# Performance work log

Hardware: AMD Instinct MI355X
Metric: run time of the kernel (lower is better)

Reference implementation:

```python
import jax, jax.numpy as jnp
import numpy as np

N_NODES = 50000


def gat_layer(x, src, dst, W, att_s, att_d, b, concat):
    # PyG GATConv (eval mode): h = x W reshaped to [N, H, C]
    H, C = att_s.shape
    h = (x @ W).reshape(-1, H, C)                      # [N, H, C]
    a_s = (h * att_s).sum(-1)                          # [N, H]
    a_d = (h * att_d).sum(-1)                          # [N, H]
    e = jax.nn.leaky_relu(a_s[src] + a_d[dst], 0.2)    # [E, H]
    # scatter-softmax over destination nodes
    m = jax.ops.segment_max(e, dst, num_segments=N_NODES)
    alpha = jnp.exp(e - m[dst])
    denom = jax.ops.segment_sum(alpha, dst, num_segments=N_NODES)
    alpha = alpha / denom[dst]                         # [E, H]
    msg = h[src] * alpha[:, :, None]                   # [E, H, C]
    out = jax.ops.segment_sum(msg, dst, num_segments=N_NODES)  # [N, H, C]
    out = out.reshape(N_NODES, H * C) if concat else out.mean(axis=1)
    return out + b


def setup_inputs() -> dict:
    key = jax.random.key(0)
    ks = jax.random.split(key, 16)
    F_IN, HID, HEADS, NCLS, E = 512, 64, 4, 40, 800000
    x = jax.random.normal(ks[0], (N_NODES, F_IN), dtype=jnp.float32)
    edge_index = jax.random.randint(ks[1], (2, E), 0, N_NODES, dtype=jnp.int32)

    def glorot(k, shape):
        fan = shape[0]
        return jax.random.normal(k, shape, dtype=jnp.float32) / np.sqrt(fan)

    d1 = HID * HEADS  # 256
    return {
        "x": x,
        "edge_index": edge_index,
        "W1": glorot(ks[2], (F_IN, d1)),
        "as1": glorot(ks[3], (HEADS, HID)),
        "ad1": glorot(ks[4], (HEADS, HID)),
        "b1": jnp.zeros((d1,), jnp.float32),
        "W2": glorot(ks[5], (d1, d1)),
        "as2": glorot(ks[6], (HEADS, HID)),
        "ad2": glorot(ks[7], (HEADS, HID)),
        "b2": jnp.zeros((d1,), jnp.float32),
        "W3": glorot(ks[8], (d1, NCLS)),
        "as3": glorot(ks[9], (1, NCLS)),
        "ad3": glorot(ks[10], (1, NCLS)),
        "b3": jnp.zeros((NCLS,), jnp.float32),
    }


def reference(x, edge_index, W1, as1, ad1, b1, W2, as2, ad2, b2, W3, as3, ad3, b3):
    # add self-loops (PyG GATConv default)
    loops = jnp.arange(N_NODES, dtype=edge_index.dtype)
    src = jnp.concatenate([edge_index[0], loops])
    dst = jnp.concatenate([edge_index[1], loops])
    h = jax.nn.elu(gat_layer(x, src, dst, W1, as1, ad1, b1, True))
    h = jax.nn.elu(gat_layer(h, src, dst, W2, as2, ad2, b2, True))
    out = gat_layer(h, src, dst, W3, as3, ad3, b3, False)
    return out
```

## Files before the change

kernel.cpp:

```cpp
#include <hip/hip_runtime.h>
#include <stdint.h>

#define NN 50000
#define NB 196

typedef unsigned short u16;
typedef _Float16 f16;
typedef __attribute__((ext_vector_type(8))) _Float16 half8;
typedef __attribute__((ext_vector_type(4))) _Float16 half4;
typedef __attribute__((ext_vector_type(4))) float f32x4;

__device__ __forceinline__ void gload_lds16(const void* gsrc, void* ldst){
  __builtin_amdgcn_global_load_lds(
      (const __attribute__((address_space(1))) unsigned int*)gsrc,
      (__attribute__((address_space(3))) unsigned int*)ldst,
      16, 0, 0);
}


__global__ void count_k(const int* __restrict__ dst, int* __restrict__ cnt, int E){
  int i = blockIdx.x * 256 + threadIdx.x;
  int tot = E + NN;
  if (i >= tot) return;
  int d = (i < E) ? dst[i] : (i - E);
  atomicAdd(&cnt[d], 1);
}

__global__ __launch_bounds__(256) void scan_part_k(const int* __restrict__ cnt,
                                                   int* __restrict__ bsum){
  __shared__ int lds[256];
  int tid = threadIdx.x;
  int idx = blockIdx.x * 256 + tid;
  lds[tid] = (idx < NN) ? cnt[idx] : 0;
  __syncthreads();
#pragma unroll
  for (int off = 128; off >= 1; off >>= 1){
    if (tid < off) lds[tid] += lds[tid + off];
    __syncthreads();
  }
  if (tid == 0) bsum[blockIdx.x] = lds[0];
}

__global__ __launch_bounds__(256) void scan_top_k(const int* __restrict__ bsum,
                                                  int* __restrict__ boff,
                                                  int* __restrict__ row_ptr){
  __shared__ int lds[256];
  int tid = threadIdx.x;
  int v = (tid < NB) ? bsum[tid] : 0;
  lds[tid] = v;
  __syncthreads();
#pragma unroll
  for (int off = 1; off < 256; off <<= 1){
    int t = (tid >= off) ? lds[tid - off] : 0;
    __syncthreads();
    lds[tid] += t;
    __syncthreads();
  }
  if (tid < NB) boff[tid] = lds[tid] - v;
  if (tid == 255) row_ptr[NN] = lds[255];
}

__global__ __launch_bounds__(256) void scan_fin_k(const int* __restrict__ cnt,
                                                  const int* __restrict__ boff,
                                                  int* __restrict__ row_ptr,
                                                  int* __restrict__ cursor){
  __shared__ int lds[256];
  int tid = threadIdx.x;
  int idx = blockIdx.x * 256 + tid;
  int v = (idx < NN) ? cnt[idx] : 0;
  lds[tid] = v;
  __syncthreads();
#pragma unroll
  for (int off = 1; off < 256; off <<= 1){
    int t = (tid >= off) ? lds[tid - off] : 0;
    __syncthreads();
    lds[tid] += t;
    __syncthreads();
  }
  if (idx < NN){
    int r = boff[blockIdx.x] + lds[tid] - v;
    row_ptr[idx] = r;
    cursor[idx]  = r;
  }
}

__global__ void scatter_k(const int* __restrict__ src, const int* __restrict__ dst,
                          int* __restrict__ cursor, int* __restrict__ csr, int E){
  int i = blockIdx.x * 256 + threadIdx.x;
  int tot = E + NN;
  if (i >= tot) return;
  int s, d;
  if (i < E){ s = src[i]; d = dst[i]; } else { s = i - E; d = i - E; }
  int pos = atomicAdd(&cursor[d], 1);
  csr[pos] = s;
}


__global__ void transpose_k(const float* __restrict__ W, f16* __restrict__ Wt, int K, int N){
  int i = blockIdx.x * 256 + threadIdx.x;
  if (i >= K * N) return;
  int n = i / K, k = i - n * K;
  Wt[i] = (f16)W[k * N + n];
}


template<bool A_FP32>
__global__ __launch_bounds__(256) void gemm_tile2_k(const void* __restrict__ Aptr,
                                                    const f16* __restrict__ Bt,
                                                    f16* __restrict__ C,
                                                    const float* __restrict__ atts,
                                                    const float* __restrict__ attd,
                                                    float* __restrict__ a_s,
                                                    float* __restrict__ a_d,
                                                    int M, int N, int K){
  constexpr int ABYTES = A_FP32 ? 16384 : 8192;
  constexpr int STEPB  = ABYTES + 8192;
  __shared__ __attribute__((aligned(16))) char lds[2 * STEPB];

  const int tid  = threadIdx.x;
  const int wave = tid >> 6, lane = tid & 63;
  const int quad = lane >> 4, l16 = lane & 15;
  const int wm = wave >> 1, wn = wave & 1;
  const int m0 = blockIdx.x * 128, n0 = blockIdx.y * 128;
  const int sc_l = lane >> 4, r_l = lane & 15;

  size_t bsrc[2]; int bdst[2];
#pragma unroll
  for (int j = 0; j < 2; ++j){
    int nt = wave * 2 + j;
    bsrc[j] = (size_t)(n0 + nt * 16 + r_l) * K + sc_l * 8;
    bdst[j] = (wave * 128 + j * 64) * 16;
  }
  size_t asrc[4]; int adst[4];
  if constexpr (A_FP32){
#pragma unroll
    for (int j = 0; j < 4; ++j){
      int mt = wave * 2 + (j & 1);
      int h  = j >> 1;
      int row = m0 + mt * 16 + r_l; if (row > M - 1) row = M - 1;
      asrc[j] = (size_t)row * K + sc_l * 8 + h * 4;
      adst[j] = h * 8192 + mt * 1024;
    }
  } else {
#pragma unroll
    for (int j = 0; j < 2; ++j){
      int mt = wave * 2 + j;
      int row = m0 + mt * 16 + r_l; if (row > M - 1) row = M - 1;
      asrc[j] = (size_t)row * K + sc_l * 8;
      adst[j] = mt * 1024;
      asrc[j + 2] = 0; adst[j + 2] = 0;
    }
  }

  auto stage = [&](int buf, int k0){
    char* Ab  = lds + buf * STEPB;
    char* Bb  = Ab + ABYTES;
    if constexpr (A_FP32){
      const float* A = (const float*)Aptr;
#pragma unroll
      for (int j = 0; j < 4; ++j)
        gload_lds16(A + asrc[j] + k0, Ab + adst[j]);
    } else {
      const f16* A = (const f16*)Aptr;
#pragma unroll
      for (int j = 0; j < 2; ++j)
        gload_lds16(A + asrc[j] + k0, Ab + adst[j]);
    }
#pragma unroll
    for (int j = 0; j < 2; ++j)
      gload_lds16(Bt + bsrc[j] + k0, Bb + bdst[j]);
  };

  f32x4 acc[4][4] = {};

  stage(0, 0);
  asm volatile("s_waitcnt vmcnt(0)" ::: "memory");
  __syncthreads();

  const int nk = K >> 5;
  int cur = 0;
  for (int t = 0; t < nk; ++t){
    if (t + 1 < nk) stage(cur ^ 1, (t + 1) << 5);

    char* Ab = lds + cur * STEPB;
    f16*  Bb = (f16*)(Ab + ABYTES);
    half8 af[4], bf[4];
    if constexpr (A_FP32){
#pragma unroll
      for (int i = 0; i < 4; ++i){
        const f32x4 lo = *(const f32x4*)(Ab + (((wm * 4 + i) * 64 + lane) * 16));
        const f32x4 hi = *(const f32x4*)(Ab + 8192 + (((wm * 4 + i) * 64 + lane) * 16));
        half8 v;
        v[0] = (f16)lo.x; v[1] = (f16)lo.y; v[2] = (f16)lo.z; v[3] = (f16)lo.w;
        v[4] = (f16)hi.x; v[5] = (f16)hi.y; v[6] = (f16)hi.z; v[7] = (f16)hi.w;
        af[i] = v;
      }
    } else {
#pragma unroll
      for (int i = 0; i < 4; ++i)
        af[i] = *(const half8*)(Ab + (((wm * 4 + i) * 64 + lane) * 16));
    }
#pragma unroll
    for (int j = 0; j < 4; ++j)
      bf[j] = *(const half8*)((char*)Bb + (((wn * 4 + j) * 64 + lane) * 16));
#pragma unroll
    for (int i = 0; i < 4; ++i)
#pragma unroll
      for (int j = 0; j < 4; ++j)
        acc[i][j] = __builtin_amdgcn_mfma_f32_16x16x32_f16(af[i], bf[j], acc[i][j], 0, 0, 0);

    __syncthreads();
    cur ^= 1;
  }

  const int head = blockIdx.y * 2 + wn;
  float sA[4], dA[4];
#pragma unroll
  for (int j = 0; j < 4; ++j){
    sA[j] = atts[head * 64 + j * 16 + l16];
    dA[j] = attd[head * 64 + j * 16 + l16];
  }
#pragma unroll
  for (int i = 0; i < 4; ++i){
#pragma unroll
    for (int r = 0; r < 4; ++r){
      int mm = m0 + (wm * 4 + i) * 16 + quad * 4 + r;
      float vs = 0.f, vd = 0.f;
#pragma unroll
      for (int j = 0; j < 4; ++j){
        float v = acc[i][j][r];
        vs += v * sA[j];
        vd += v * dA[j];
        int n = n0 + (wn * 4 + j) * 16 + l16;
        if (mm < M) C[(size_t)mm * N + n] = (f16)v;
      }
#pragma unroll
      for (int off = 8; off >= 1; off >>= 1){
        vs += __shfl_xor(vs, off);
        vd += __shfl_xor(vd, off);
      }
      if (l16 == 0 && mm < M){
        a_s[mm * 4 + head] = vs;
        a_d[mm * 4 + head] = vd;
      }
    }
  }
}


__global__ __launch_bounds__(256) void gemm_k(const f16* __restrict__ A,
                                              const f16* __restrict__ Bt,
                                              f16* __restrict__ C,
                                              const float* __restrict__ atts,
                                              const float* __restrict__ attd,
                                              float* __restrict__ a_s,
                                              float* __restrict__ a_d,
                                              int M, int N, int K){
  __shared__ f16 As[64 * 40];
  __shared__ f16 Bs[64 * 40];
  const int tid  = threadIdx.x;
  const int wave = tid >> 6, lane = tid & 63;
  const int quad = lane >> 4, l16 = lane & 15;
  const int m0 = blockIdx.x * 64, n0 = blockIdx.y * 64;
  const int srow = tid >> 2;
  const int scol = (tid & 3) * 8;

  f32x4 acc[4] = {};

  for (int k0 = 0; k0 < K; k0 += 32){
    half8 va = {0,0,0,0,0,0,0,0};
    int gm = m0 + srow;
    if (gm < M) va = *(const half8*)(A + (size_t)gm * K + k0 + scol);
    *(half8*)(&As[srow * 40 + scol]) = va;

    half8 vb = {0,0,0,0,0,0,0,0};
    int gn = n0 + srow;
    if (gn < N) vb = *(const half8*)(Bt + (size_t)gn * K + k0 + scol);
    *(half8*)(&Bs[srow * 40 + scol]) = vb;

    __syncthreads();
    half8 af = *(const half8*)(&As[(wave * 16 + l16) * 40 + quad * 8]);
#pragma unroll
    for (int i = 0; i < 4; i++){
      half8 bf = *(const half8*)(&Bs[(i * 16 + l16) * 40 + quad * 8]);
      acc[i] = __builtin_amdgcn_mfma_f32_16x16x32_f16(af, bf, acc[i], 0, 0, 0);
    }
    __syncthreads();
  }

#pragma unroll
  for (int i = 0; i < 4; i++){
    int n = n0 + i * 16 + l16;
#pragma unroll
    for (int r = 0; r < 4; r++){
      int m = m0 + wave * 16 + quad * 4 + r;
      if (m < M && n < N) C[(size_t)m * N + n] = (f16)acc[i][r];
    }
  }

  float sA[4], dA[4];
#pragma unroll
  for (int i = 0; i < 4; i++){
    int n = n0 + i * 16 + l16;
    sA[i] = (n < N) ? atts[n] : 0.f;
    dA[i] = (n < N) ? attd[n] : 0.f;
  }
#pragma unroll
  for (int r = 0; r < 4; r++){
    float vs = 0.f, vd = 0.f;
#pragma unroll
    for (int i = 0; i < 4; i++){
      vs += acc[i][r] * sA[i];
      vd += acc[i][r] * dA[i];
    }
#pragma unroll
    for (int off = 8; off >= 1; off >>= 1){
      vs += __shfl_xor(vs, off);
      vd += __shfl_xor(vd, off);
    }
    int m = m0 + wave * 16 + quad * 4 + r;
    if (l16 == 0 && m < M){
      a_s[m] = vs;
      a_d[m] = vd;
    }
  }
}


__device__ __forceinline__ float lrelu(float e){ return e > 0.f ? e : 0.2f * e; }

__global__ __launch_bounds__(256) void agg4_k(const f16* __restrict__ h,
                                              const float* __restrict__ a_s,
                                              const float* __restrict__ a_d,
                                              const int* __restrict__ row_ptr,
                                              const int* __restrict__ csr,
                                              const float* __restrict__ bias,
                                              f16* __restrict__ out){
  int w = blockIdx.x * 4 + (threadIdx.x >> 6);
  if (w >= NN) return;
  int lane = threadIdx.x & 63;
  int head = lane >> 4;
  float ad = a_d[w * 4 + head];
  int beg = row_ptr[w], end = row_ptr[w + 1];

  float m = -1e30f, denom = 0.f;
  float acc0 = 0.f, acc1 = 0.f, acc2 = 0.f, acc3 = 0.f;

  int s0 = csr[beg];
  int s1 = csr[(beg + 1 < end) ? beg + 1 : beg];
  float e0 = a_s[s0 * 4 + head];
  float e1 = a_s[s1 * 4 + head];
  half4 h0 = *(const half4*)(h + (size_t)s0 * 256 + lane * 4);
  half4 h1 = *(const half4*)(h + (size_t)s1 * 256 + lane * 4);

  for (int j = beg; j < end; j += 2){
    int t0 = (j + 2 < end) ? j + 2 : j;
    int t1 = (j + 3 < end) ? j + 3 : j;
    int sp0 = csr[t0], sp1 = csr[t1];
    float ep0 = a_s[sp0 * 4 + head];
    float ep1 = a_s[sp1 * 4 + head];
    half4 hp0 = *(const half4*)(h + (size_t)sp0 * 256 + lane * 4);
    half4 hp1 = *(const half4*)(h + (size_t)sp1 * 256 + lane * 4);

    float ee0 = lrelu(e0 + ad);
    float ee1 = (j + 1 < end) ? lrelu(e1 + ad) : -1e30f;
    float mn = fmaxf(m, fmaxf(ee0, ee1));
    float cold = __expf(m - mn);
    float al0 = __expf(ee0 - mn);
    float al1 = __expf(ee1 - mn);
    denom = denom * cold + al0 + al1;
    acc0 = acc0 * cold + al0 * (float)h0.x + al1 * (float)h1.x;
    acc1 = acc1 * cold + al0 * (float)h0.y + al1 * (float)h1.y;
    acc2 = acc2 * cold + al0 * (float)h0.z + al1 * (float)h1.z;
    acc3 = acc3 * cold + al0 * (float)h0.w + al1 * (float)h1.w;
    m = mn;
    e0 = ep0; e1 = ep1; h0 = hp0; h1 = hp1;
  }

  float inv = 1.f / fmaxf(denom, 1e-30f);
  float o0 = acc0 * inv + bias[lane * 4 + 0];
  float o1 = acc1 * inv + bias[lane * 4 + 1];
  float o2 = acc2 * inv + bias[lane * 4 + 2];
  float o3 = acc3 * inv + bias[lane * 4 + 3];
  o0 = o0 > 0.f ? o0 : __expf(o0) - 1.f;
  o1 = o1 > 0.f ? o1 : __expf(o1) - 1.f;
  o2 = o2 > 0.f ? o2 : __expf(o2) - 1.f;
  o3 = o3 > 0.f ? o3 : __expf(o3) - 1.f;
  half4 r; r.x = (f16)o0; r.y = (f16)o1; r.z = (f16)o2; r.w = (f16)o3;
  *(half4*)(out + (size_t)w * 256 + lane * 4) = r;
}

__global__ __launch_bounds__(256) void agg1_k(const f16* __restrict__ h,
                                              const float* __restrict__ a_s,
                                              const float* __restrict__ a_d,
                                              const int* __restrict__ row_ptr,
                                              const int* __restrict__ csr,
                                              const float* __restrict__ bias,
                                              float* __restrict__ out){
  int w = blockIdx.x * 4 + (threadIdx.x >> 6);
  if (w >= NN) return;
  int lane = threadIdx.x & 63;
  int cl = (lane < 40) ? lane : 0;
  float ad = a_d[w];
  int beg = row_ptr[w], end = row_ptr[w + 1];

  float m = -1e30f, denom = 0.f, acc = 0.f;

  int s0 = csr[beg];
  int s1 = csr[(beg + 1 < end) ? beg + 1 : beg];
  float e0 = a_s[s0];
  float e1 = a_s[s1];
  float h0 = (float)h[(size_t)s0 * 40 + cl];
  float h1 = (float)h[(size_t)s1 * 40 + cl];

  for (int j = beg; j < end; j += 2){
    int t0 = (j + 2 < end) ? j + 2 : j;
    int t1 = (j + 3 < end) ? j + 3 : j;
    int sp0 = csr[t0], sp1 = csr[t1];
    float ep0 = a_s[sp0];
    float ep1 = a_s[sp1];
    float hp0 = (float)h[(size_t)sp0 * 40 + cl];
    float hp1 = (float)h[(size_t)sp1 * 40 + cl];

    float ee0 = lrelu(e0 + ad);
    float ee1 = (j + 1 < end) ? lrelu(e1 + ad) : -1e30f;
    float mn = fmaxf(m, fmaxf(ee0, ee1));
    float cold = __expf(m - mn);
    float al0 = __expf(ee0 - mn);
    float al1 = __expf(ee1 - mn);
    denom = denom * cold + al0 + al1;
    acc = acc * cold + al0 * h0 + al1 * h1;
    m = mn;
    e0 = ep0; e1 = ep1; h0 = hp0; h1 = hp1;
  }

  if (lane < 40){
    float o = acc / fmaxf(denom, 1e-30f) + bias[lane];
    out[(size_t)w * 40 + lane] = o;
  }
}


extern "C" void kernel_launch(void* const* d_in, const int* in_sizes, int n_in,
                              void* d_out, int out_size, void* d_ws, size_t ws_size,
                              hipStream_t stream){
  const float* x   = (const float*)d_in[0];
  const int*   ei  = (const int*)d_in[1];
  const float* W1  = (const float*)d_in[2];
  const float* as1 = (const float*)d_in[3];
  const float* ad1 = (const float*)d_in[4];
  const float* b1  = (const float*)d_in[5];
  const float* W2  = (const float*)d_in[6];
  const float* as2 = (const float*)d_in[7];
  const float* ad2 = (const float*)d_in[8];
  const float* b2  = (const float*)d_in[9];
  const float* W3  = (const float*)d_in[10];
  const float* as3 = (const float*)d_in[11];
  const float* ad3 = (const float*)d_in[12];
  const float* b3  = (const float*)d_in[13];

  const int E = in_sizes[1] / 2;
  const int ETOT = E + NN;
  const int* src_arr = ei;
  const int* dst_arr = ei + E;

  char* ws = (char*)d_ws;
  size_t off = 0;
  auto alloc = [&](size_t bytes) -> void* {
    void* p = ws + off; off += (bytes + 255) & ~(size_t)255; return p;
  };
  int*   cnt     = (int*)  alloc((size_t)NN * 4);
  int*   row_ptr = (int*)  alloc((size_t)(NN + 1) * 4);
  int*   cursor  = (int*)  alloc((size_t)NN * 4);
  int*   csr     = (int*)  alloc((size_t)ETOT * 4);
  int*   bsum    = (int*)  alloc((size_t)256 * 4);
  int*   boff    = (int*)  alloc((size_t)256 * 4);
  f16*   W1t     = (f16*)  alloc((size_t)512 * 256 * 2);
  f16*   W2t     = (f16*)  alloc((size_t)256 * 256 * 2);
  f16*   W3t     = (f16*)  alloc((size_t)256 * 40 * 2);
  float* a_s     = (float*)alloc((size_t)NN * 4 * 4);
  float* a_d     = (float*)alloc((size_t)NN * 4 * 4);
  f16*   hbuf    = (f16*)  alloc((size_t)NN * 256 * 2);
  f16*   xbuf    = (f16*)  alloc((size_t)NN * 256 * 2);
  (void)ws_size; (void)n_in; (void)out_size;

  hipMemsetAsync(cnt, 0, (size_t)NN * 4, stream);
  int egrid = (ETOT + 255) / 256;
  count_k    <<<egrid, 256, 0, stream>>>(dst_arr, cnt, E);
  scan_part_k<<<NB, 256, 0, stream>>>(cnt, bsum);
  scan_top_k <<<1, 256, 0, stream>>>(bsum, boff, row_ptr);
  scan_fin_k <<<NB, 256, 0, stream>>>(cnt, boff, row_ptr, cursor);
  scatter_k  <<<egrid, 256, 0, stream>>>(src_arr, dst_arr, cursor, csr, E);

  transpose_k<<<(512 * 256 + 255) / 256, 256, 0, stream>>>(W1, W1t, 512, 256);
  transpose_k<<<(256 * 256 + 255) / 256, 256, 0, stream>>>(W2, W2t, 256, 256);
  transpose_k<<<(256 * 40  + 255) / 256, 256, 0, stream>>>(W3, W3t, 256, 40);

  dim3 blk(256);
  dim3 gT((NN + 127) / 128, 2);
  dim3 gC((NN + 63) / 64, 1);
  int nodeblocks = (NN + 3) / 4;

  gemm_tile2_k<true> <<<gT, blk, 0, stream>>>(x, W1t, hbuf, as1, ad1, a_s, a_d, NN, 256, 512);
  agg4_k <<<nodeblocks, blk, 0, stream>>>(hbuf, a_s, a_d, row_ptr, csr, b1, xbuf);

  gemm_tile2_k<false><<<gT, blk, 0, stream>>>(xbuf, W2t, hbuf, as2, ad2, a_s, a_d, NN, 256, 256);
  agg4_k <<<nodeblocks, blk, 0, stream>>>(hbuf, a_s, a_d, row_ptr, csr, b2, xbuf);

  gemm_k<<<gC, blk, 0, stream>>>(xbuf, W3t, hbuf, as3, ad3, a_s, a_d, NN, 40, 256);
  agg1_k <<<nodeblocks, blk, 0, stream>>>(hbuf, a_s, a_d, row_ptr, csr, b3, (float*)d_out);
}
```

Baseline: 549.7 us.

## Retile GEMMs, add pipelined N=40 GEMM, drop online max in aggregation

After: 534.1 us. 2.8% less time.

```diff
diff --git a/kernel.cpp b/kernel.cpp
--- a/kernel.cpp
+++ b/kernel.cpp
@@ -105,7 +105,7 @@
 
 
 template<bool A_FP32>
-__global__ __launch_bounds__(256) void gemm_tile2_k(const void* __restrict__ Aptr,
+__global__ __launch_bounds__(512) void gemm_tile3_k(const void* __restrict__ Aptr,
                                                     const f16* __restrict__ Bt,
                                                     f16* __restrict__ C,
                                                     const float* __restrict__ atts,
@@ -113,7 +113,7 @@
                                                     float* __restrict__ a_s,
                                                     float* __restrict__ a_d,
                                                     int M, int N, int K){
-  constexpr int ABYTES = A_FP32 ? 16384 : 8192;
+  constexpr int ABYTES = A_FP32 ? 8192 : 4096;
   constexpr int STEPB  = ABYTES + 8192;
   __shared__ __attribute__((aligned(16))) char lds[2 * STEPB];
 
@@ -121,57 +121,38 @@
   const int wave = tid >> 6, lane = tid & 63;
   const int quad = lane >> 4, l16 = lane & 15;
   const int wm = wave >> 1, wn = wave & 1;
-  const int m0 = blockIdx.x * 128, n0 = blockIdx.y * 128;
+  const int m0 = blockIdx.x * 64, n0 = blockIdx.y * 128;
   const int sc_l = lane >> 4, r_l = lane & 15;
 
-  size_t bsrc[2]; int bdst[2];
-#pragma unroll
-  for (int j = 0; j < 2; ++j){
-    int nt = wave * 2 + j;
-    bsrc[j] = (size_t)(n0 + nt * 16 + r_l) * K + sc_l * 8;
-    bdst[j] = (wave * 128 + j * 64) * 16;
-  }
-  size_t asrc[4]; int adst[4];
-  if constexpr (A_FP32){
-#pragma unroll
-    for (int j = 0; j < 4; ++j){
-      int mt = wave * 2 + (j & 1);
-      int h  = j >> 1;
-      int row = m0 + mt * 16 + r_l; if (row > M - 1) row = M - 1;
-      asrc[j] = (size_t)row * K + sc_l * 8 + h * 4;
-      adst[j] = h * 8192 + mt * 1024;
-    }
-  } else {
-#pragma unroll
-    for (int j = 0; j < 2; ++j){
-      int mt = wave * 2 + j;
-      int row = m0 + mt * 16 + r_l; if (row > M - 1) row = M - 1;
-      asrc[j] = (size_t)row * K + sc_l * 8;
-      adst[j] = mt * 1024;
-      asrc[j + 2] = 0; adst[j + 2] = 0;
+  size_t bsrc = (size_t)(n0 + wave * 16 + r_l) * K + sc_l * 8;
+  const int bdst = wave * 1024;
+  size_t asrc; int adst; bool a_active = true;
+  {
+    int mt = wave & 3;
+    int row = m0 + mt * 16 + r_l; if (row > M - 1) row = M - 1;
+    if constexpr (A_FP32){
+      int hp = wave >> 2;
+      asrc = (size_t)row * K + sc_l * 8 + hp * 4;
+      adst = hp * 4096 + mt * 1024;
+    } else {
+      asrc = (size_t)row * K + sc_l * 8;
+      adst = mt * 1024;
+      a_active = (wave < 4);
     }
   }
 
   auto stage = [&](int buf, int k0){
-    char* Ab  = lds + buf * STEPB;
-    char* Bb  = Ab + ABYTES;
+    char* Ab = lds + buf * STEPB;
+    char* Bb = Ab + ABYTES;
     if constexpr (A_FP32){
-      const float* A = (const float*)Aptr;
-#pragma unroll
-      for (int j = 0; j < 4; ++j)
-        gload_lds16(A + asrc[j] + k0, Ab + adst[j]);
+      gload_lds16((const float*)Aptr + asrc + k0, Ab + adst);
     } else {
-      const f16* A = (const f16*)Aptr;
-#pragma unroll
-      for (int j = 0; j < 2; ++j)
-        gload_lds16(A + asrc[j] + k0, Ab + adst[j]);
-    }
-#pragma unroll
-    for (int j = 0; j < 2; ++j)
-      gload_lds16(Bt + bsrc[j] + k0, Bb + bdst[j]);
+      if (a_active) gload_lds16((const f16*)Aptr + asrc + k0, Ab + adst);
+    }
+    gload_lds16(Bt + bsrc + k0, Bb + bdst);
   };
 
-  f32x4 acc[4][4] = {};
+  f32x4 acc[4] = {};
 
   stage(0, 0);
   asm volatile("s_waitcnt vmcnt(0)" ::: "memory");
@@ -183,31 +164,23 @@
     if (t + 1 < nk) stage(cur ^ 1, (t + 1) << 5);
 
     char* Ab = lds + cur * STEPB;
-    f16*  Bb = (f16*)(Ab + ABYTES);
-    half8 af[4], bf[4];
+    char* Bb = Ab + ABYTES;
+    half8 af;
     if constexpr (A_FP32){
-#pragma unroll
-      for (int i = 0; i < 4; ++i){
-        const f32x4 lo = *(const f32x4*)(Ab + (((wm * 4 + i) * 64 + lane) * 16));
-        const f32x4 hi = *(const f32x4*)(Ab + 8192 + (((wm * 4 + i) * 64 + lane) * 16));
-        half8 v;
-        v[0] = (f16)lo.x; v[1] = (f16)lo.y; v[2] = (f16)lo.z; v[3] = (f16)lo.w;
-        v[4] = (f16)hi.x; v[5] = (f16)hi.y; v[6] = (f16)hi.z; v[7] = (f16)hi.w;
-        af[i] = v;
-      }
+      const f32x4 lo = *(const f32x4*)(Ab + (wm * 64 + lane) * 16);
+      const f32x4 hi = *(const f32x4*)(Ab + 4096 + (wm * 64 + lane) * 16);
+      af[0] = (f16)lo.x; af[1] = (f16)lo.y; af[2] = (f16)lo.z; af[3] = (f16)lo.w;
+      af[4] = (f16)hi.x; af[5] = (f16)hi.y; af[6] = (f16)hi.z; af[7] = (f16)hi.w;
     } else {
-#pragma unroll
-      for (int i = 0; i < 4; ++i)
-        af[i] = *(const half8*)(Ab + (((wm * 4 + i) * 64 + lane) * 16));
-    }
+      af = *(const half8*)(Ab + (wm * 64 + lane) * 16);
+    }
+    half8 bf[4];
 #pragma unroll
     for (int j = 0; j < 4; ++j)
-      bf[j] = *(const half8*)((char*)Bb + (((wn * 4 + j) * 64 + lane) * 16));
-#pragma unroll
-    for (int i = 0; i < 4; ++i)
-#pragma unroll
-      for (int j = 0; j < 4; ++j)
-        acc[i][j] = __builtin_amdgcn_mfma_f32_16x16x32_f16(af[i], bf[j], acc[i][j], 0, 0, 0);
+      bf[j] = *(const half8*)(Bb + ((wn * 4 + j) * 64 + lane) * 16);
+#pragma unroll
+    for (int j = 0; j < 4; ++j)
+      acc[j] = __builtin_amdgcn_mfma_f32_16x16x32_f16(af, bf[j], acc[j], 0, 0, 0);
 
     __syncthreads();
     cur ^= 1;
@@ -221,107 +194,114 @@
     dA[j] = attd[head * 64 + j * 16 + l16];
   }
 #pragma unroll
-  for (int i = 0; i < 4; ++i){
-#pragma unroll
-    for (int r = 0; r < 4; ++r){
-      int mm = m0 + (wm * 4 + i) * 16 + quad * 4 + r;
-      float vs = 0.f, vd = 0.f;
-#pragma unroll
-      for (int j = 0; j < 4; ++j){
-        float v = acc[i][j][r];
-        vs += v * sA[j];
-        vd += v * dA[j];
-        int n = n0 + (wn * 4 + j) * 16 + l16;
-        if (mm < M) C[(size_t)mm * N + n] = (f16)v;
-      }
-#pragma unroll
-      for (int off = 8; off >= 1; off >>= 1){
-        vs += __shfl_xor(vs, off);
-        vd += __shfl_xor(vd, off);
-      }
-      if (l16 == 0 && mm < M){
-        a_s[mm * 4 + head] = vs;
-        a_d[mm * 4 + head] = vd;
-      }
-    }
-  }
-}
-
-
-__global__ __launch_bounds__(256) void gemm_k(const f16* __restrict__ A,
-                                              const f16* __restrict__ Bt,
-                                              f16* __restrict__ C,
-                                              const float* __restrict__ atts,
-                                              const float* __restrict__ attd,
-                                              float* __restrict__ a_s,
-                                              float* __restrict__ a_d,
-                                              int M, int N, int K){
-  __shared__ f16 As[64 * 40];
-  __shared__ f16 Bs[64 * 40];
+  for (int r = 0; r < 4; ++r){
+    int mm = m0 + wm * 16 + quad * 4 + r;
+    float vs = 0.f, vd = 0.f;
+#pragma unroll
+    for (int j = 0; j < 4; ++j){
+      float v = acc[j][r];
+      vs += v * sA[j];
+      vd += v * dA[j];
+      int n = n0 + (wn * 4 + j) * 16 + l16;
+      if (mm < M) C[(size_t)mm * N + n] = (f16)v;
+    }
+#pragma unroll
+    for (int off = 8; off >= 1; off >>= 1){
+      vs += __shfl_xor(vs, off);
+      vd += __shfl_xor(vd, off);
+    }
+    if (l16 == 0 && mm < M){
+      a_s[mm * 4 + head] = vs;
+      a_d[mm * 4 + head] = vd;
+    }
+  }
+}
+
+
+__global__ __launch_bounds__(256) void gemm_n40_k(const f16* __restrict__ A,
+                                                  const f16* __restrict__ Bt,
+                                                  f16* __restrict__ C,
+                                                  const float* __restrict__ atts,
+                                                  const float* __restrict__ attd,
+                                                  float* __restrict__ a_s,
+                                                  float* __restrict__ a_d,
+                                                  int M, int K){
+  constexpr int ABYTES = 4096;
+  constexpr int BBYTES = 3072;
+  constexpr int STEPB  = ABYTES + BBYTES;
+  __shared__ __attribute__((aligned(16))) char lds[2 * STEPB];
+
   const int tid  = threadIdx.x;
   const int wave = tid >> 6, lane = tid & 63;
   const int quad = lane >> 4, l16 = lane & 15;
-  const int m0 = blockIdx.x * 64, n0 = blockIdx.y * 64;
-  const int srow = tid >> 2;
-  const int scol = (tid & 3) * 8;
-
-  f32x4 acc[4] = {};
-
-  for (int k0 = 0; k0 < K; k0 += 32){
-    half8 va = {0,0,0,0,0,0,0,0};
-    int gm = m0 + srow;
-    if (gm < M) va = *(const half8*)(A + (size_t)gm * K + k0 + scol);
-    *(half8*)(&As[srow * 40 + scol]) = va;
-
-    half8 vb = {0,0,0,0,0,0,0,0};
-    int gn = n0 + srow;
-    if (gn < N) vb = *(const half8*)(Bt + (size_t)gn * K + k0 + scol);
-    *(half8*)(&Bs[srow * 40 + scol]) = vb;
-
-    __syncthreads();
-    half8 af = *(const half8*)(&As[(wave * 16 + l16) * 40 + quad * 8]);
-#pragma unroll
-    for (int i = 0; i < 4; i++){
-      half8 bf = *(const half8*)(&Bs[(i * 16 + l16) * 40 + quad * 8]);
-      acc[i] = __builtin_amdgcn_mfma_f32_16x16x32_f16(af, bf, acc[i], 0, 0, 0);
-    }
-    __syncthreads();
-  }
-
-#pragma unroll
-  for (int i = 0; i < 4; i++){
-    int n = n0 + i * 16 + l16;
-#pragma unroll
-    for (int r = 0; r < 4; r++){
-      int m = m0 + wave * 16 + quad * 4 + r;
-      if (m < M && n < N) C[(size_t)m * N + n] = (f16)acc[i][r];
-    }
-  }
-
-  float sA[4], dA[4];
-#pragma unroll
-  for (int i = 0; i < 4; i++){
-    int n = n0 + i * 16 + l16;
-    sA[i] = (n < N) ? atts[n] : 0.f;
-    dA[i] = (n < N) ? attd[n] : 0.f;
-  }
-#pragma unroll
-  for (int r = 0; r < 4; r++){
+  const int m0 = blockIdx.x * 64;
+  const int sc_l = lane >> 4, r_l = lane & 15;
+
+  int arow = m0 + wave * 16 + r_l; if (arow > M - 1) arow = M - 1;
+  const size_t asrc = (size_t)arow * K + sc_l * 8;
+  const int adst = wave * 1024;
+  int brow = wave * 16 + r_l; if (brow > 39) brow = 39;
+  const size_t bsrc = (size_t)brow * K + sc_l * 8;
+  const int bdst = wave * 1024;
+  const bool b_active = (wave < 3);
+
+  auto stage = [&](int buf, int k0){
+    char* Ab = lds + buf * STEPB;
+    char* Bb = Ab + ABYTES;
+    gload_lds16(A + asrc + k0, Ab + adst);
+    if (b_active) gload_lds16(Bt + bsrc + k0, Bb + bdst);
+  };
+
+  f32x4 acc[3] = {};
+  stage(0, 0);
+  asm volatile("s_waitcnt vmcnt(0)" ::: "memory");
+  __syncthreads();
+
+  const int nk = K >> 5;
+  int cur = 0;
+  for (int t = 0; t < nk; ++t){
+    if (t + 1 < nk) stage(cur ^ 1, (t + 1) << 5);
+    char* Ab = lds + cur * STEPB;
+    char* Bb = Ab + ABYTES;
+    half8 af = *(const half8*)(Ab + (wave * 64 + lane) * 16);
+    half8 bf[3];
+#pragma unroll
+    for (int j = 0; j < 3; ++j)
+      bf[j] = *(const half8*)(Bb + (j * 64 + lane) * 16);
+#pragma unroll
+    for (int j = 0; j < 3; ++j)
+      acc[j] = __builtin_amdgcn_mfma_f32_16x16x32_f16(af, bf[j], acc[j], 0, 0, 0);
+    __syncthreads();
+    cur ^= 1;
+  }
+
+  float sA[3], dA[3];
+#pragma unroll
+  for (int j = 0; j < 3; ++j){
+    int n = j * 16 + l16;
+    sA[j] = (n < 40) ? atts[n] : 0.f;
+    dA[j] = (n < 40) ? attd[n] : 0.f;
+  }
+#pragma unroll
+  for (int r = 0; r < 4; ++r){
+    int mm = m0 + wave * 16 + quad * 4 + r;
     float vs = 0.f, vd = 0.f;
 #pragma unroll
-    for (int i = 0; i < 4; i++){
-      vs += acc[i][r] * sA[i];
-      vd += acc[i][r] * dA[i];
+    for (int j = 0; j < 3; ++j){
+      float v = acc[j][r];
+      vs += v * sA[j];
+      vd += v * dA[j];
+      int n = j * 16 + l16;
+      if (mm < M && n < 40) C[(size_t)mm * 40 + n] = (f16)v;
     }
 #pragma unroll
     for (int off = 8; off >= 1; off >>= 1){
       vs += __shfl_xor(vs, off);
       vd += __shfl_xor(vd, off);
     }
-    int m = m0 + wave * 16 + quad * 4 + r;
-    if (l16 == 0 && m < M){
-      a_s[m] = vs;
-      a_d[m] = vd;
+    if (l16 == 0 && mm < M){
+      a_s[mm] = vs;
+      a_d[mm] = vd;
     }
   }
 }
@@ -338,43 +318,48 @@
                                               f16* __restrict__ out){
   int w = blockIdx.x * 4 + (threadIdx.x >> 6);
   if (w >= NN) return;
-  int lane = threadIdx.x & 63;
-  int head = lane >> 4;
-  float ad = a_d[w * 4 + head];
-  int beg = row_ptr[w], end = row_ptr[w + 1];
-
-  float m = -1e30f, denom = 0.f;
-  float acc0 = 0.f, acc1 = 0.f, acc2 = 0.f, acc3 = 0.f;
-
-  int s0 = csr[beg];
-  int s1 = csr[(beg + 1 < end) ? beg + 1 : beg];
-  float e0 = a_s[s0 * 4 + head];
-  float e1 = a_s[s1 * 4 + head];
-  half4 h0 = *(const half4*)(h + (size_t)s0 * 256 + lane * 4);
-  half4 h1 = *(const half4*)(h + (size_t)s1 * 256 + lane * 4);
-
-  for (int j = beg; j < end; j += 2){
-    int t0 = (j + 2 < end) ? j + 2 : j;
-    int t1 = (j + 3 < end) ? j + 3 : j;
-    int sp0 = csr[t0], sp1 = csr[t1];
-    float ep0 = a_s[sp0 * 4 + head];
-    float ep1 = a_s[sp1 * 4 + head];
-    half4 hp0 = *(const half4*)(h + (size_t)sp0 * 256 + lane * 4);
-    half4 hp1 = *(const half4*)(h + (size_t)sp1 * 256 + lane * 4);
-
-    float ee0 = lrelu(e0 + ad);
-    float ee1 = (j + 1 < end) ? lrelu(e1 + ad) : -1e30f;
-    float mn = fmaxf(m, fmaxf(ee0, ee1));
-    float cold = __expf(m - mn);
-    float al0 = __expf(ee0 - mn);
-    float al1 = __expf(ee1 - mn);
-    denom = denom * cold + al0 + al1;
-    acc0 = acc0 * cold + al0 * (float)h0.x + al1 * (float)h1.x;
-    acc1 = acc1 * cold + al0 * (float)h0.y + al1 * (float)h1.y;
-    acc2 = acc2 * cold + al0 * (float)h0.z + al1 * (float)h1.z;
-    acc3 = acc3 * cold + al0 * (float)h0.w + al1 * (float)h1.w;
-    m = mn;
-    e0 = ep0; e1 = ep1; h0 = hp0; h1 = hp1;
+  const int lane = threadIdx.x & 63;
+  const int head = lane >> 4;
+  const char* hb = (const char*)h;
+  const uint32_t hoff_lane = (uint32_t)lane << 3;
+  const float ad = a_d[w * 4 + head];
+  const int beg = row_ptr[w], end = row_ptr[w + 1], endm1 = end - 1;
+
+  float denom = 0.f, acc0 = 0.f, acc1 = 0.f, acc2 = 0.f, acc3 = 0.f;
+
+  float ce[4]; half4 chv[4];
+  float ne[4]; half4 nhv[4];
+
+  auto ldgrp = [&](int base, float* EV, half4* HV){
+#pragma unroll
+    for (int q = 0; q < 4; ++q){
+      int idx = base + q; idx = idx < endm1 ? idx : endm1;
+      int s = csr[idx];
+      EV[q] = a_s[(s << 2) + head];
+      HV[q] = *(const half4*)(hb + (((uint32_t)s << 9) | hoff_lane));
+    }
+  };
+
+  ldgrp(beg, ce, chv);
+  int base = beg;
+  while (true){
+    bool more = base + 4 < end;
+    if (more) ldgrp(base + 4, ne, nhv);
+    int rem = end - base;
+#pragma unroll
+    for (int q = 0; q < 4; ++q){
+      float al = __expf(lrelu(ce[q] + ad));
+      al = (q < rem) ? al : 0.f;
+      denom += al;
+      acc0 += al * (float)chv[q].x;
+      acc1 += al * (float)chv[q].y;
+      acc2 += al * (float)chv[q].z;
+      acc3 += al * (float)chv[q].w;
+    }
+    if (!more) break;
+#pragma unroll
+    for (int q = 0; q < 4; ++q){ ce[q] = ne[q]; chv[q] = nhv[q]; }
+    base += 4;
   }
 
   float inv = 1.f / fmaxf(denom, 1e-30f);
@@ -399,39 +384,42 @@
                                               float* __restrict__ out){
   int w = blockIdx.x * 4 + (threadIdx.x >> 6);
   if (w >= NN) return;
-  int lane = threadIdx.x & 63;
-  int cl = (lane < 40) ? lane : 0;
-  float ad = a_d[w];
-  int beg = row_ptr[w], end = row_ptr[w + 1];
-
-  float m = -1e30f, denom = 0.f, acc = 0.f;
-
-  int s0 = csr[beg];
-  int s1 = csr[(beg + 1 < end) ? beg + 1 : beg];
-  float e0 = a_s[s0];
-  float e1 = a_s[s1];
-  float h0 = (float)h[(size_t)s0 * 40 + cl];
-  float h1 = (float)h[(size_t)s1 * 40 + cl];
-
-  for (int j = beg; j < end; j += 2){
-    int t0 = (j + 2 < end) ? j + 2 : j;
-    int t1 = (j + 3 < end) ? j + 3 : j;
-    int sp0 = csr[t0], sp1 = csr[t1];
-    float ep0 = a_s[sp0];
-    float ep1 = a_s[sp1];
-    float hp0 = (float)h[(size_t)sp0 * 40 + cl];
-    float hp1 = (float)h[(size_t)sp1 * 40 + cl];
-
-    float ee0 = lrelu(e0 + ad);
-    float ee1 = (j + 1 < end) ? lrelu(e1 + ad) : -1e30f;
-    float mn = fmaxf(m, fmaxf(ee0, ee1));
-    float cold = __expf(m - mn);
-    float al0 = __expf(ee0 - mn);
-    float al1 = __expf(ee1 - mn);
-    denom = denom * cold + al0 + al1;
-    acc = acc * cold + al0 * h0 + al1 * h1;
-    m = mn;
-    e0 = ep0; e1 = ep1; h0 = hp0; h1 = hp1;
+  const int lane = threadIdx.x & 63;
+  const int cl = (lane < 40) ? lane : 0;
+  const float ad = a_d[w];
+  const int beg = row_ptr[w], end = row_ptr[w + 1], endm1 = end - 1;
+
+  float denom = 0.f, acc = 0.f;
+  float ce[4], chv[4];
+  float ne[4], nhv[4];
+
+  auto ldgrp = [&](int base, float* EV, float* HV){
+#pragma unroll
+    for (int q = 0; q < 4; ++q){
+      int idx = base + q; idx = idx < endm1 ? idx : endm1;
+      int s = csr[idx];
+      EV[q] = a_s[s];
+      HV[q] = (float)h[(size_t)s * 40 + cl];
+    }
+  };
+
+  ldgrp(beg, ce, chv);
+  int base = beg;
+  while (true){
+    bool more = base + 4 < end;
+    if (more) ldgrp(base + 4, ne, nhv);
+    int rem = end - base;
+#pragma unroll
+    for (int q = 0; q < 4; ++q){
+      float al = __expf(lrelu(ce[q] + ad));
+      al = (q < rem) ? al : 0.f;
+      denom += al;
+      acc += al * chv[q];
+    }
+    if (!more) break;
+#pragma unroll
+    for (int q = 0; q < 4; ++q){ ce[q] = ne[q]; chv[q] = nhv[q]; }
+    base += 4;
   }
 
   if (lane < 40){
@@ -496,17 +484,18 @@
   transpose_k<<<(256 * 256 + 255) / 256, 256, 0, stream>>>(W2, W2t, 256, 256);
   transpose_k<<<(256 * 40  + 255) / 256, 256, 0, stream>>>(W3, W3t, 256, 40);
 
+  dim3 blk512(512);
   dim3 blk(256);
-  dim3 gT((NN + 127) / 128, 2);
+  dim3 gT((NN + 63) / 64, 2);
   dim3 gC((NN + 63) / 64, 1);
   int nodeblocks = (NN + 3) / 4;
 
-  gemm_tile2_k<true> <<<gT, blk, 0, stream>>>(x, W1t, hbuf, as1, ad1, a_s, a_d, NN, 256, 512);
+  gemm_tile3_k<true> <<<gT, blk512, 0, stream>>>(x, W1t, hbuf, as1, ad1, a_s, a_d, NN, 256, 512);
   agg4_k <<<nodeblocks, blk, 0, stream>>>(hbuf, a_s, a_d, row_ptr, csr, b1, xbuf);
 
-  gemm_tile2_k<false><<<gT, blk, 0, stream>>>(xbuf, W2t, hbuf, as2, ad2, a_s, a_d, NN, 256, 256);
+  gemm_tile3_k<false><<<gT, blk512, 0, stream>>>(xbuf, W2t, hbuf, as2, ad2, a_s, a_d, NN, 256, 256);
   agg4_k <<<nodeblocks, blk, 0, stream>>>(hbuf, a_s, a_d, row_ptr, csr, b2, xbuf);
 
-  gemm_k<<<gC, blk, 0, stream>>>(xbuf, W3t, hbuf, as3, ad3, a_s, a_d, NN, 40, 256);
+  gemm_n40_k<<<gC, blk, 0, stream>>>(xbuf, W3t, hbuf, as3, ad3, a_s, a_d, NN, 256);
   agg1_k <<<nodeblocks, blk, 0, stream>>>(hbuf, a_s, a_d, row_ptr, csr, b3, (float*)d_out);
 }
```
